# Kernel optimization log

Hardware: AMD Instinct MI355X
Metric: run time of the kernel (lower is better)

Reference implementation:

```python
import jax, jax.numpy as jnp
import numpy as np

# Router hyperparameters (match init_kwargs)
GATE_TEMP = 1.0
Z_LOSS_COEF = 0.01
CAPACITY_FACTOR = 1.25
NUM_SELECTED = 2
NUM_EXPERTS = 64

B, S, D = 4, 8192, 2048


def setup_inputs() -> dict:
    key = jax.random.key(0)
    k1, k2 = jax.random.split(key)
    hidden_states = jax.random.normal(k1, (B, S, D), dtype=jnp.float32)
    # nn.init.normal_(self.gate.weight, mean=0.0, std=0.01)
    gate_weight = jax.random.normal(k2, (NUM_EXPERTS, D), dtype=jnp.float32) * 0.01
    return {"hidden_states": hidden_states, "gate_weight": gate_weight}


def reference(hidden_states, gate_weight):
    b, s, d = hidden_states.shape
    e = gate_weight.shape[0]
    n = b * s  # num_tokens
    x = hidden_states.reshape(n, d)

    # gate linear (no bias), eval mode -> no jitter noise
    gate_logits = (x @ gate_weight.T) / GATE_TEMP          # [n, e]
    gate_probs = jax.nn.softmax(gate_logits, axis=-1)      # [n, e]

    top_k_probs, top_k_indices = jax.lax.top_k(gate_probs, NUM_SELECTED)  # [n, k]
    expert_weights = top_k_probs / (top_k_probs.sum(-1, keepdims=True) + 1e-8)

    # capacity accounting (vectorized bincount instead of per-expert python loop;
    # top-k indices are distinct per token so `any(dim=-1)` == plain count)
    capacity = int(CAPACITY_FACTOR * n / e * NUM_SELECTED)
    expert_counts = jnp.zeros((e,), jnp.float32).at[top_k_indices.reshape(-1)].add(1.0)
    expert_overflow = jnp.maximum(expert_counts - capacity, 0.0).sum()
    capacity_overflow_pct = expert_overflow / n * 100.0

    # auxiliary metrics
    z_loss = jax.scipy.special.logsumexp(gate_logits, axis=-1).mean() * Z_LOSS_COEF
    gate_entropy = -(gate_probs * jnp.log(gate_probs + 1e-10)).sum(-1).mean()
    expert_load = expert_counts / expert_counts.sum()
    expert_load_variance = ((expert_load - 1.0 / e) ** 2).mean()
    routing_confidence = expert_weights.max(-1)  # [n]

    expert_indices = top_k_indices.reshape(b, s, NUM_SELECTED)
    expert_weights = expert_weights.reshape(b, s, NUM_SELECTED)
    return (expert_indices, expert_weights, expert_counts, capacity_overflow_pct,
            z_loss, gate_entropy, expert_load_variance,
            routing_confidence.reshape(b, s))
```

## Files before the change

kernel.cpp:

```cpp
#include <hip/hip_runtime.h>


#define NTOK 32768
#define DDIM 2048
#define NEXP 64
#define NKS 64
#define LG_STRIDE 68

#define OFF_IDX 0
#define OFF_W 65536
#define OFF_CNT 131072
#define OFF_OVF 131136
#define OFF_ZL 131137
#define OFF_ENT 131138
#define OFF_VAR 131139
#define OFF_CONF 131140

#define WS_PLANES_OFF 1024
#define WS_NEEDED (WS_PLANES_OFF + NKS * 8192)

struct RouterWS {
  unsigned int counts[NEXP];
  double z_sum;
  double ent_sum;
};

typedef _Float16 half8 __attribute__((ext_vector_type(8)));
typedef float floatx4 __attribute__((ext_vector_type(4)));

typedef __attribute__((address_space(1))) void v1_t;
typedef __attribute__((address_space(3))) void v3_t;
__device__ __forceinline__ void cp16(const void* g, void* l) {
  __builtin_amdgcn_global_load_lds((v1_t*)g, (v3_t*)l, 16, 0, 0);
}

__global__ void convert_w(const float* __restrict__ w, _Float16* __restrict__ wp) {
  int tid = blockIdx.x * 256 + threadIdx.x;
  int l = tid & 63;
  int t = (tid >> 6) & 3;
  int s = tid >> 8;
  int e = 16 * t + (l & 15);
  int k0 = 32 * s + (l >> 4) * 8;
  const float* src = w + (size_t)e * DDIM + k0;
  half8 h, lo;
#pragma unroll
  for (int i = 0; i < 8; ++i) {
    float v = src[i] * 256.0f;
    _Float16 hh = (_Float16)v;
    h[i] = hh;
    lo[i] = (_Float16)(v - (float)hh);
  }
  size_t base = (size_t)s * 4096 + ((size_t)t * 64 + l) * 8;
  *(half8*)(wp + base) = h;
  *(half8*)(wp + base + 2048) = lo;
}

__global__ __launch_bounds__(256, 2) void router_mfma(
    const float* __restrict__ x, const _Float16* __restrict__ wp,
    float* __restrict__ out, RouterWS* __restrict__ ws) {
  __shared__ _Float16 wlds[2 * 4096];
  __shared__ float lg[64 * LG_STRIDE];
  __shared__ unsigned int hist[NEXP];

  const int tid = threadIdx.x;
  const int l = tid & 63;
  const int wv = __builtin_amdgcn_readfirstlane(tid >> 6);
  const int r = l & 15;
  const int g = l >> 4;

  const int tokb = blockIdx.x * 64;
  const float* xrow = x + (size_t)(tokb + wv * 16 + r) * DDIM + g * 8;

  floatx4 acc[4];
#pragma unroll
  for (int t = 0; t < 4; ++t) {
    floatx4 z = {0.f, 0.f, 0.f, 0.f};
    acc[t] = z;
  }

  float4 xA0 = *(const float4*)(xrow + 0);
  float4 xA1 = *(const float4*)(xrow + 4);
  float4 xB0 = *(const float4*)(xrow + 32);
  float4 xB1 = *(const float4*)(xrow + 36);
  cp16(wp + tid * 8, (void*)&wlds[tid * 8]);
  cp16(wp + 2048 + tid * 8, (void*)&wlds[2048 + tid * 8]);
  __syncthreads();

#define CVT8(X0, X1, XH, XL)                                                   \
  {                                                                            \
    float vv[8] = {X0.x, X0.y, X0.z, X0.w, X1.x, X1.y, X1.z, X1.w};            \
    _Pragma("unroll") for (int i = 0; i < 8; ++i) {                            \
      _Float16 hh = (_Float16)vv[i];                                           \
      XH[i] = hh;                                                              \
      XL[i] = (_Float16)(vv[i] - (float)hh);                                   \
    }                                                                          \
  }

#define STEP(S, CB, NB, X0, X1)                                                \
  {                                                                            \
    const int s_ = (S);                                                        \
    if (s_ + 1 < NKS) {         \
      const _Float16* sp = wp + (size_t)(s_ + 1) * 4096 + tid * 8;             \
      cp16(sp, (void*)&wlds[(NB) + tid * 8]);                                  \
      cp16(sp + 2048, (void*)&wlds[(NB) + 2048 + tid * 8]);                    \
    }                                                                          \
    half8 xh, xl;                                                              \
    CVT8(X0, X1, xh, xl);                                                      \
    if (s_ + 2 < NKS) {           \
      X0 = *(const float4*)(xrow + (s_ + 2) * 32);                             \
      X1 = *(const float4*)(xrow + (s_ + 2) * 32 + 4);                         \
    }                                                                          \
    _Pragma("unroll") for (int t = 0; t < 4; ++t) {                            \
      half8 wh = *(const half8*)&wlds[(CB) + (t * 64 + l) * 8];                \
      half8 wl = *(const half8*)&wlds[(CB) + 2048 + (t * 64 + l) * 8];         \
      acc[t] = __builtin_amdgcn_mfma_f32_16x16x32_f16(xh, wh, acc[t], 0, 0, 0);\
      acc[t] = __builtin_amdgcn_mfma_f32_16x16x32_f16(xh, wl, acc[t], 0, 0, 0);\
      acc[t] = __builtin_amdgcn_mfma_f32_16x16x32_f16(xl, wh, acc[t], 0, 0, 0);\
      acc[t] = __builtin_amdgcn_mfma_f32_16x16x32_f16(xl, wl, acc[t], 0, 0, 0);\
    }                                                                          \
    __syncthreads();                                                           \
  }

  for (int ss = 0; ss < NKS; ss += 2) {
    STEP(ss, 0, 4096, xA0, xA1);
    STEP(ss + 1, 4096, 0, xB0, xB1);
  }
#undef STEP
#undef CVT8

#pragma unroll
  for (int t = 0; t < 4; ++t)
#pragma unroll
    for (int j = 0; j < 4; ++j)
      lg[(wv * 16 + g * 4 + j) * LG_STRIDE + 16 * t + r] = acc[t][j] * 0.00390625f;

  if (tid < NEXP) hist[tid] = 0;
  __syncthreads();

  if (tid < 64) {
    const int t = tid;
    const float* Lg = &lg[t * LG_STRIDE];

    float m1 = Lg[0];
    int i1 = 0;
    for (int e = 1; e < NEXP; ++e) {
      float v = Lg[e];
      if (v > m1) { m1 = v; i1 = e; }
    }
    float m2 = -3.4e38f;
    int i2 = 0;
    for (int e = 0; e < NEXP; ++e) {
      if (e == i1) continue;
      float v = Lg[e];
      if (v > m2) { m2 = v; i2 = e; }
    }

    float s = 0.f;
    for (int e = 0; e < NEXP; ++e) s += expf(Lg[e] - m1);
    float p1 = expf(Lg[i1] - m1) / s;
    float p2 = expf(Lg[i2] - m1) / s;
    float wsum = p1 + p2 + 1e-8f;
    float w1 = p1 / wsum;
    float w2 = p2 / wsum;

    float ent = 0.f;
    for (int e = 0; e < NEXP; ++e) {
      float p = expf(Lg[e] - m1) / s;
      ent -= p * logf(p + 1e-10f);
    }
    float lse = m1 + logf(s);

    size_t gt = (size_t)blockIdx.x * 64 + t;
    out[OFF_IDX + gt * 2 + 0] = (float)i1;
    out[OFF_IDX + gt * 2 + 1] = (float)i2;
    out[OFF_W + gt * 2 + 0] = w1;
    out[OFF_W + gt * 2 + 1] = w2;
    out[OFF_CONF + gt] = fmaxf(w1, w2);

    atomicAdd(&hist[i1], 1u);
    atomicAdd(&hist[i2], 1u);

    float zv = lse, ev = ent;
#pragma unroll
    for (int o = 32; o > 0; o >>= 1) {
      zv += __shfl_down(zv, o);
      ev += __shfl_down(ev, o);
    }
    if (t == 0) {
      atomicAdd(&ws->z_sum, (double)zv);
      atomicAdd(&ws->ent_sum, (double)ev);
    }
  }
  __syncthreads();
  if (tid < NEXP) atomicAdd(&ws->counts[tid], hist[tid]);
}

#define TTILE 128
#define KB 32
#define NCH (DDIM / KB)
#define XSTR 36
#define XBUF (TTILE * XSTR)
#define WBUF (NEXP * XSTR)
#define WOFF (2 * XBUF)

__global__ __launch_bounds__(512, 4) void router_fp32(
    const float* __restrict__ x, const float* __restrict__ w,
    float* __restrict__ out, RouterWS* __restrict__ ws) {
  __shared__ float smem[2 * XBUF + 2 * WBUF];
  __shared__ unsigned int hist[NEXP];

  const int tid = threadIdx.x;
  const int L = tid & 63;
  const int wv = __builtin_amdgcn_readfirstlane(tid >> 6);
  const float* xg = x + (size_t)blockIdx.x * TTILE * DDIM;
  const int sr = tid >> 3;
  const int sc = (tid & 7) * 4;

  float4 rx0 = *(const float4*)(xg + (size_t)sr * DDIM + sc);
  float4 rx1 = *(const float4*)(xg + (size_t)(sr + 64) * DDIM + sc);
  float4 rw = *(const float4*)(w + (size_t)sr * DDIM + sc);
  *(float4*)&smem[sr * XSTR + sc] = rx0;
  *(float4*)&smem[(sr + 64) * XSTR + sc] = rx1;
  *(float4*)&smem[WOFF + sr * XSTR + sc] = rw;

  float acc0[8], acc1[8];
#pragma unroll
  for (int e = 0; e < 8; ++e) { acc0[e] = 0.f; acc1[e] = 0.f; }
  __syncthreads();

  for (int c = 0; c < NCH; ++c) {
    const int cxb = (c & 1) * XBUF;
    const int cwb = WOFF + (c & 1) * WBUF;
    if (c + 1 < NCH) {
      int k0 = (c + 1) * KB;
      rx0 = *(const float4*)(xg + (size_t)sr * DDIM + k0 + sc);
      rx1 = *(const float4*)(xg + (size_t)(sr + 64) * DDIM + k0 + sc);
      rw = *(const float4*)(w + (size_t)sr * DDIM + k0 + sc);
    }
    float4 xr0[8], xr1[8];
#pragma unroll
    for (int m = 0; m < 8; ++m) {
      xr0[m] = *(const float4*)&smem[cxb + L * XSTR + 4 * m];
      xr1[m] = *(const float4*)&smem[cxb + (L + 64) * XSTR + 4 * m];
    }
#pragma unroll
    for (int e = 0; e < 8; ++e) {
      const float* wrow = &smem[cwb + (8 * wv + e) * XSTR];
      float a0 = acc0[e], a1 = acc1[e];
#pragma unroll
      for (int m = 0; m < 8; ++m) {
        float4 wq = *(const float4*)&wrow[4 * m];
        a0 = fmaf(xr0[m].x, wq.x, a0);
        a0 = fmaf(xr0[m].y, wq.y, a0);
        a0 = fmaf(xr0[m].z, wq.z, a0);
        a0 = fmaf(xr0[m].w, wq.w, a0);
        a1 = fmaf(xr1[m].x, wq.x, a1);
        a1 = fmaf(xr1[m].y, wq.y, a1);
        a1 = fmaf(xr1[m].z, wq.z, a1);
        a1 = fmaf(xr1[m].w, wq.w, a1);
      }
      acc0[e] = a0;
      acc1[e] = a1;
    }
    if (c + 1 < NCH) {
      const int nxb = ((c + 1) & 1) * XBUF;
      const int nwb = WOFF + ((c + 1) & 1) * WBUF;
      *(float4*)&smem[nxb + sr * XSTR + sc] = rx0;
      *(float4*)&smem[nxb + (sr + 64) * XSTR + sc] = rx1;
      *(float4*)&smem[nwb + sr * XSTR + sc] = rw;
    }
    __syncthreads();
  }

#pragma unroll
  for (int e = 0; e < 8; ++e) {
    smem[L * LG_STRIDE + wv * 8 + e] = acc0[e];
    smem[(L + 64) * LG_STRIDE + wv * 8 + e] = acc1[e];
  }
  if (tid < NEXP) hist[tid] = 0;
  __syncthreads();

  if (tid < TTILE) {
    const int t = tid;
    const float* Lg = &smem[t * LG_STRIDE];
    float m1 = Lg[0];
    int i1 = 0;
    for (int e = 1; e < NEXP; ++e) {
      float v = Lg[e];
      if (v > m1) { m1 = v; i1 = e; }
    }
    float m2 = -3.4e38f;
    int i2 = 0;
    for (int e = 0; e < NEXP; ++e) {
      if (e == i1) continue;
      float v = Lg[e];
      if (v > m2) { m2 = v; i2 = e; }
    }
    float s = 0.f;
    for (int e = 0; e < NEXP; ++e) s += expf(Lg[e] - m1);
    float p1 = expf(Lg[i1] - m1) / s;
    float p2 = expf(Lg[i2] - m1) / s;
    float wsum = p1 + p2 + 1e-8f;
    float w1 = p1 / wsum;
    float w2 = p2 / wsum;
    float ent = 0.f;
    for (int e = 0; e < NEXP; ++e) {
      float p = expf(Lg[e] - m1) / s;
      ent -= p * logf(p + 1e-10f);
    }
    float lse = m1 + logf(s);
    size_t gt = (size_t)blockIdx.x * TTILE + t;
    out[OFF_IDX + gt * 2 + 0] = (float)i1;
    out[OFF_IDX + gt * 2 + 1] = (float)i2;
    out[OFF_W + gt * 2 + 0] = w1;
    out[OFF_W + gt * 2 + 1] = w2;
    out[OFF_CONF + gt] = fmaxf(w1, w2);
    atomicAdd(&hist[i1], 1u);
    atomicAdd(&hist[i2], 1u);
    float zv = lse, ev = ent;
#pragma unroll
    for (int o = 32; o > 0; o >>= 1) {
      zv += __shfl_down(zv, o);
      ev += __shfl_down(ev, o);
    }
    if ((tid & 63) == 0) {
      atomicAdd(&ws->z_sum, (double)zv);
      atomicAdd(&ws->ent_sum, (double)ev);
    }
  }
  __syncthreads();
  if (tid < NEXP) atomicAdd(&ws->counts[tid], hist[tid]);
}

__global__ void router_final(float* __restrict__ out, RouterWS* __restrict__ ws) {
  int e = threadIdx.x;
  float c = (float)ws->counts[e];
  out[OFF_CNT + e] = c;
  float over = fmaxf(c - 1280.f, 0.f);
  float ld = c / 65536.f - (1.f / 64.f);
  float so = over, sv = ld * ld;
#pragma unroll
  for (int o = 32; o > 0; o >>= 1) {
    so += __shfl_down(so, o);
    sv += __shfl_down(sv, o);
  }
  if (e == 0) {
    out[OFF_OVF] = so / 32768.f * 100.f;
    out[OFF_VAR] = sv / 64.f;
    out[OFF_ZL] = (float)(ws->z_sum / 32768.0 * 0.01);
    out[OFF_ENT] = (float)(ws->ent_sum / 32768.0);
  }
}

extern "C" void kernel_launch(void* const* d_in, const int* in_sizes, int n_in,
                              void* d_out, int out_size, void* d_ws, size_t ws_size,
                              hipStream_t stream) {
  const float* x = (const float*)d_in[0];
  const float* w = (const float*)d_in[1];
  float* out = (float*)d_out;
  RouterWS* ws = (RouterWS*)d_ws;

  (void)hipMemsetAsync(d_ws, 0, sizeof(RouterWS), stream);
  if (ws_size >= (size_t)WS_NEEDED) {
    _Float16* wp = (_Float16*)((char*)d_ws + WS_PLANES_OFF);
    hipLaunchKernelGGL(convert_w, dim3(64), dim3(256), 0, stream, w, wp);
    hipLaunchKernelGGL(router_mfma, dim3(NTOK / 64), dim3(256), 0, stream,
                       x, wp, out, ws);
  } else {
    hipLaunchKernelGGL(router_fp32, dim3(NTOK / TTILE), dim3(512), 0, stream,
                       x, w, out, ws);
  }
  hipLaunchKernelGGL(router_final, dim3(1), dim3(64), 0, stream, out, ws);
}
```

Measured before the change: 89.61 us.

## Load gate weights directly into registers and drop per-step LDS barriers

Instead of staging each K-slice of the packed fp16 weights into LDS with global_load_lds and synchronizing the block every step, each wave now loads its weight fragments straight from global memory into registers, double-buffered across steps. This removes the per-step __syncthreads and the LDS traffic. In exchange, every wave issues its own global loads of the shared weight slice, giving four times the L2/L1 weight traffic, and the two register buffers add about 64 VGPRs, which may strain the launch bound of 2 blocks per CU.

New measurement: 105.0 us. 17.1% more time.

```diff
diff --git a/kernel.cpp b/kernel.cpp
--- a/kernel.cpp
+++ b/kernel.cpp
@@ -27,12 +27,6 @@
 
 typedef _Float16 half8 __attribute__((ext_vector_type(8)));
 typedef float floatx4 __attribute__((ext_vector_type(4)));
-
-typedef __attribute__((address_space(1))) void v1_t;
-typedef __attribute__((address_space(3))) void v3_t;
-__device__ __forceinline__ void cp16(const void* g, void* l) {
-  __builtin_amdgcn_global_load_lds((v1_t*)g, (v3_t*)l, 16, 0, 0);
-}
 
 __global__ void convert_w(const float* __restrict__ w, _Float16* __restrict__ wp) {
   int tid = blockIdx.x * 256 + threadIdx.x;
@@ -58,7 +52,6 @@
 __global__ __launch_bounds__(256, 2) void router_mfma(
     const float* __restrict__ x, const _Float16* __restrict__ wp,
     float* __restrict__ out, RouterWS* __restrict__ ws) {
-  __shared__ _Float16 wlds[2 * 4096];
   __shared__ float lg[64 * LG_STRIDE];
   __shared__ unsigned int hist[NEXP];
 
@@ -70,6 +63,7 @@
 
   const int tokb = blockIdx.x * 64;
   const float* xrow = x + (size_t)(tokb + wv * 16 + r) * DDIM + g * 8;
+  const _Float16* wl8 = wp + (size_t)l * 8;
 
   floatx4 acc[4];
 #pragma unroll
@@ -82,9 +76,12 @@
   float4 xA1 = *(const float4*)(xrow + 4);
   float4 xB0 = *(const float4*)(xrow + 32);
   float4 xB1 = *(const float4*)(xrow + 36);
-  cp16(wp + tid * 8, (void*)&wlds[tid * 8]);
-  cp16(wp + 2048 + tid * 8, (void*)&wlds[2048 + tid * 8]);
-  __syncthreads();
+  half8 wA[8], wB[8];
+#pragma unroll
+  for (int t = 0; t < 4; ++t) {
+    wA[2 * t] = *(const half8*)(wl8 + t * 512);
+    wA[2 * t + 1] = *(const half8*)(wl8 + 2048 + t * 512);
+  }
 
 #define CVT8(X0, X1, XH, XL)                                                   \
   {                                                                            \
@@ -96,13 +93,15 @@
     }                                                                          \
   }
 
-#define STEP(S, CB, NB, X0, X1)                                                \
+#define STEP(S, WCUR, WNXT, X0, X1)                                            \
   {                                                                            \
     const int s_ = (S);                                                        \
-    if (s_ + 1 < NKS) {         \
-      const _Float16* sp = wp + (size_t)(s_ + 1) * 4096 + tid * 8;             \
-      cp16(sp, (void*)&wlds[(NB) + tid * 8]);                                  \
-      cp16(sp + 2048, (void*)&wlds[(NB) + 2048 + tid * 8]);                    \
+    if (s_ + 1 < NKS) {      \
+      const _Float16* sp = wl8 + (size_t)(s_ + 1) * 4096;                      \
+      _Pragma("unroll") for (int t = 0; t < 4; ++t) {                          \
+        WNXT[2 * t] = *(const half8*)(sp + t * 512);                           \
+        WNXT[2 * t + 1] = *(const half8*)(sp + 2048 + t * 512);                \
+      }                                                                        \
     }                                                                          \
     half8 xh, xl;                                                              \
     CVT8(X0, X1, xh, xl);                                                      \
@@ -110,20 +109,21 @@
       X0 = *(const float4*)(xrow + (s_ + 2) * 32);                             \
       X1 = *(const float4*)(xrow + (s_ + 2) * 32 + 4);                         \
     }                                                                          \
-    _Pragma("unroll") for (int t = 0; t < 4; ++t) {                            \
-      half8 wh = *(const half8*)&wlds[(CB) + (t * 64 + l) * 8];                \
-      half8 wl = *(const half8*)&wlds[(CB) + 2048 + (t * 64 + l) * 8];         \
-      acc[t] = __builtin_amdgcn_mfma_f32_16x16x32_f16(xh, wh, acc[t], 0, 0, 0);\
-      acc[t] = __builtin_amdgcn_mfma_f32_16x16x32_f16(xh, wl, acc[t], 0, 0, 0);\
-      acc[t] = __builtin_amdgcn_mfma_f32_16x16x32_f16(xl, wh, acc[t], 0, 0, 0);\
-      acc[t] = __builtin_amdgcn_mfma_f32_16x16x32_f16(xl, wl, acc[t], 0, 0, 0);\
+    _Pragma("unroll") for (int t = 0; t < 4; ++t) {     \
+      acc[t] = __builtin_amdgcn_mfma_f32_16x16x32_f16(xh, WCUR[2 * t],         \
+                                                      acc[t], 0, 0, 0);        \
+      acc[t] = __builtin_amdgcn_mfma_f32_16x16x32_f16(xh, WCUR[2 * t + 1],     \
+                                                      acc[t], 0, 0, 0);        \
+      acc[t] = __builtin_amdgcn_mfma_f32_16x16x32_f16(xl, WCUR[2 * t],         \
+                                                      acc[t], 0, 0, 0);        \
+      acc[t] = __builtin_amdgcn_mfma_f32_16x16x32_f16(xl, WCUR[2 * t + 1],     \
+                                                      acc[t], 0, 0, 0);        \
     }                                                                          \
-    __syncthreads();                                                           \
   }
 
   for (int ss = 0; ss < NKS; ss += 2) {
-    STEP(ss, 0, 4096, xA0, xA1);
-    STEP(ss + 1, 4096, 0, xB0, xB1);
+    STEP(ss, wA, wB, xA0, xA1);
+    STEP(ss + 1, wB, wA, xB0, xB1);
   }
 #undef STEP
 #undef CVT8
```

## Stage x tiles through swizzled LDS with a 4-deep async copy pipeline

Applied to the files above, without the earlier changes.

Activations were previously loaded straight from global memory into registers, two k-steps ahead. They are now copied asynchronously into LDS next to the weight planes, using an XOR-swizzled layout, inside a 4-buffer ring that prefetches 3 stages ahead. Each stage ends with an explicit vmcnt wait plus barrier instead of __syncthreads. The goal is to keep more memory loads in flight and hide global latency for the bandwidth-bound x stream. In exchange, LDS use grows to 64KB per block, which may cap occupancy below the 2 blocks per CU requested by the launch bounds.

Result: faster. 75.12 us, median of 2 (-16.2%).

```diff
diff --git a/kernel.cpp b/kernel.cpp
--- a/kernel.cpp
+++ b/kernel.cpp
@@ -58,8 +58,7 @@
 __global__ __launch_bounds__(256, 2) void router_mfma(
     const float* __restrict__ x, const _Float16* __restrict__ wp,
     float* __restrict__ out, RouterWS* __restrict__ ws) {
-  __shared__ _Float16 wlds[2 * 4096];
-  __shared__ float lg[64 * LG_STRIDE];
+  __shared__ __align__(16) char smem[65536];
   __shared__ unsigned int hist[NEXP];
 
   const int tid = threadIdx.x;
@@ -69,7 +68,19 @@
   const int g = l >> 4;
 
   const int tokb = blockIdx.x * 64;
-  const float* xrow = x + (size_t)(tokb + wv * 16 + r) * DDIM + g * 8;
+  const float* xg = x + (size_t)tokb * DDIM;
+
+  const int srow0 = tid >> 3;
+  const int srow1 = srow0 + 32;
+  const int sj = tid & 7;
+  const size_t gx0 = (size_t)srow0 * DDIM + 4 * (sj ^ (srow0 & 7));
+  const size_t gx1 = (size_t)srow1 * DDIM + 4 * (sj ^ (srow1 & 7));
+
+  const int row = wv * 16 + r;
+  const int rs = row & 7;
+  const int so0 = 16 * (row * 8 + ((2 * g) ^ rs));
+  const int so1 = 16 * (row * 8 + ((2 * g + 1) ^ rs));
+  const int wlo = 16 * l;
 
   floatx4 acc[4];
 #pragma unroll
@@ -78,13 +89,19 @@
     acc[t] = z;
   }
 
-  float4 xA0 = *(const float4*)(xrow + 0);
-  float4 xA1 = *(const float4*)(xrow + 4);
-  float4 xB0 = *(const float4*)(xrow + 32);
-  float4 xB1 = *(const float4*)(xrow + 36);
-  cp16(wp + tid * 8, (void*)&wlds[tid * 8]);
-  cp16(wp + 2048 + tid * 8, (void*)&wlds[2048 + tid * 8]);
-  __syncthreads();
+#define STAGE(S, BUF)                                                          \
+  {                                                                            \
+    char* bb_ = smem + (BUF) * 16384;                                          \
+    cp16(xg + (size_t)(S) * 32 + gx0, bb_ + tid * 16);                         \
+    cp16(xg + (size_t)(S) * 32 + gx1, bb_ + 4096 + tid * 16);                  \
+    const char* wsrc_ = (const char*)wp + (size_t)(S) * 8192 + tid * 16;       \
+    cp16(wsrc_, bb_ + 8192 + tid * 16);                                        \
+    cp16(wsrc_ + 4096, bb_ + 12288 + tid * 16);                                \
+  }
+
+#define WAITBAR(NW)                                                            \
+  asm volatile("s_waitcnt vmcnt(" #NW ")\n\ts_barrier" ::: "memory");          \
+  __builtin_amdgcn_sched_barrier(0);
 
 #define CVT8(X0, X1, XH, XL)                                                   \
   {                                                                            \
@@ -96,45 +113,66 @@
     }                                                                          \
   }
 
-#define STEP(S, CB, NB, X0, X1)                                                \
+#define COMPUTE(BUF)                                                           \
+  const char* bb = smem + (BUF) * 16384;                                       \
+  float4 xq0 = *(const float4*)(bb + so0);                                     \
+  float4 xq1 = *(const float4*)(bb + so1);                                     \
+  half8 xh, xl;                                                                \
+  CVT8(xq0, xq1, xh, xl);                                                      \
+  _Pragma("unroll") for (int t = 0; t < 4; ++t) {                              \
+    half8 wh = *(const half8*)(bb + 8192 + 1024 * t + wlo);                    \
+    half8 wl = *(const half8*)(bb + 12288 + 1024 * t + wlo);                   \
+    acc[t] = __builtin_amdgcn_mfma_f32_16x16x32_f16(xh, wh, acc[t], 0, 0, 0);  \
+    acc[t] = __builtin_amdgcn_mfma_f32_16x16x32_f16(xh, wl, acc[t], 0, 0, 0);  \
+    acc[t] = __builtin_amdgcn_mfma_f32_16x16x32_f16(xl, wh, acc[t], 0, 0, 0);  \
+    acc[t] = __builtin_amdgcn_mfma_f32_16x16x32_f16(xl, wl, acc[t], 0, 0, 0);  \
+  }
+
+#define STEP(S, BUF, NW)                                                       \
   {                                                                            \
-    const int s_ = (S);                                                        \
-    if (s_ + 1 < NKS) {         \
-      const _Float16* sp = wp + (size_t)(s_ + 1) * 4096 + tid * 8;             \
-      cp16(sp, (void*)&wlds[(NB) + tid * 8]);                                  \
-      cp16(sp + 2048, (void*)&wlds[(NB) + 2048 + tid * 8]);                    \
-    }                                                                          \
-    half8 xh, xl;                                                              \
-    CVT8(X0, X1, xh, xl);                                                      \
-    if (s_ + 2 < NKS) {           \
-      X0 = *(const float4*)(xrow + (s_ + 2) * 32);                             \
-      X1 = *(const float4*)(xrow + (s_ + 2) * 32 + 4);                         \
-    }                                                                          \
-    _Pragma("unroll") for (int t = 0; t < 4; ++t) {                            \
-      half8 wh = *(const half8*)&wlds[(CB) + (t * 64 + l) * 8];                \
-      half8 wl = *(const half8*)&wlds[(CB) + 2048 + (t * 64 + l) * 8];         \
-      acc[t] = __builtin_amdgcn_mfma_f32_16x16x32_f16(xh, wh, acc[t], 0, 0, 0);\
-      acc[t] = __builtin_amdgcn_mfma_f32_16x16x32_f16(xh, wl, acc[t], 0, 0, 0);\
-      acc[t] = __builtin_amdgcn_mfma_f32_16x16x32_f16(xl, wh, acc[t], 0, 0, 0);\
-      acc[t] = __builtin_amdgcn_mfma_f32_16x16x32_f16(xl, wl, acc[t], 0, 0, 0);\
-    }                                                                          \
-    __syncthreads();                                                           \
-  }
-
-  for (int ss = 0; ss < NKS; ss += 2) {
-    STEP(ss, 0, 4096, xA0, xA1);
-    STEP(ss + 1, 4096, 0, xB0, xB1);
-  }
+    STAGE((S) + 3, (((S) + 3) & 3));                                           \
+    COMPUTE(BUF)                                                               \
+    WAITBAR(NW)                                                                \
+  }
+#define STEPN(S, BUF, NW)                                  \
+  {                                                                            \
+    COMPUTE(BUF)                                                               \
+    WAITBAR(NW)                                                                \
+  }
+
+  STAGE(0, 0)
+  STAGE(1, 1)
+  STAGE(2, 2)
+  if (tid < NEXP) hist[tid] = 0;
+  WAITBAR(8)
+
+  for (int ss = 0; ss < 60; ss += 4) {
+    STEP(ss, 0, 8)
+    STEP(ss + 1, 1, 8)
+    STEP(ss + 2, 2, 8)
+    STEP(ss + 3, 3, 8)
+  }
+  STEP(60, 0, 8)
+  STEPN(61, 1, 4)
+  STEPN(62, 2, 0)
+  {
+    COMPUTE(3)
+  }
+  __syncthreads();
+
 #undef STEP
+#undef STEPN
+#undef COMPUTE
 #undef CVT8
-
+#undef WAITBAR
+#undef STAGE
+
+  float* lg = (float*)smem;
 #pragma unroll
   for (int t = 0; t < 4; ++t)
 #pragma unroll
     for (int j = 0; j < 4; ++j)
       lg[(wv * 16 + g * 4 + j) * LG_STRIDE + 16 * t + r] = acc[t][j] * 0.00390625f;
-
-  if (tid < NEXP) hist[tid] = 0;
   __syncthreads();
 
   if (tid < 64) {
```

## Deepen weight staging to a 4-buffer pipeline with explicit vmcnt waits

Applied to the files above, without the earlier changes.

Replaces the double-buffered LDS weight staging with a four-slot ring buffer that prefetches three K-steps ahead. Each step ends with a hand-written s_waitcnt on a chosen vmcnt plus s_barrier, so the wait covers only the oldest loads and not all outstanding ones. The logits scratch now reuses the same LDS region, keeping LDS use within the 2-blocks-per-CU budget. This adds latency hiding for the global-to-LDS copies. It relies on exact counts of outstanding vector memory operations, which is fragile if the compiler reorders or splits loads.

New measurement: 82.29 us. 8.2% less time.

```diff
diff --git a/kernel.cpp b/kernel.cpp
--- a/kernel.cpp
+++ b/kernel.cpp
@@ -58,8 +58,7 @@
 __global__ __launch_bounds__(256, 2) void router_mfma(
     const float* __restrict__ x, const _Float16* __restrict__ wp,
     float* __restrict__ out, RouterWS* __restrict__ ws) {
-  __shared__ _Float16 wlds[2 * 4096];
-  __shared__ float lg[64 * LG_STRIDE];
+  __shared__ __align__(16) char smem[32768];
   __shared__ unsigned int hist[NEXP];
 
   const int tid = threadIdx.x;
@@ -70,6 +69,7 @@
 
   const int tokb = blockIdx.x * 64;
   const float* xrow = x + (size_t)(tokb + wv * 16 + r) * DDIM + g * 8;
+  const int wlo = 16 * l;
 
   floatx4 acc[4];
 #pragma unroll
@@ -78,13 +78,25 @@
     acc[t] = z;
   }
 
-  float4 xA0 = *(const float4*)(xrow + 0);
-  float4 xA1 = *(const float4*)(xrow + 4);
-  float4 xB0 = *(const float4*)(xrow + 32);
-  float4 xB1 = *(const float4*)(xrow + 36);
-  cp16(wp + tid * 8, (void*)&wlds[tid * 8]);
-  cp16(wp + 2048 + tid * 8, (void*)&wlds[2048 + tid * 8]);
-  __syncthreads();
+  float4 xA0, xA1, xB0, xB1;
+
+#define XLOAD(S, X0, X1)                                                       \
+  {                                                                            \
+    X0 = *(const float4*)(xrow + (size_t)(S) * 32);                            \
+    X1 = *(const float4*)(xrow + (size_t)(S) * 32 + 4);                        \
+  }
+
+#define WSTAGE(S, WB)                                                          \
+  {                                                                            \
+    char* bb_ = smem + (WB) * 8192;                                            \
+    const char* ws_ = (const char*)wp + (size_t)(S) * 8192 + tid * 16;         \
+    cp16(ws_, bb_ + tid * 16);                                                 \
+    cp16(ws_ + 4096, bb_ + 4096 + tid * 16);                                   \
+  }
+
+#define WAITBAR(NW)                                                            \
+  asm volatile("s_waitcnt vmcnt(" #NW ")\n\ts_barrier" ::: "memory");          \
+  __builtin_amdgcn_sched_barrier(0);
 
 #define CVT8(X0, X1, XH, XL)                                                   \
   {                                                                            \
@@ -96,45 +108,81 @@
     }                                                                          \
   }
 
-#define STEP(S, CB, NB, X0, X1)                                                \
+#define MFMAS(WB, XH, XL)                                                      \
   {                                                                            \
-    const int s_ = (S);                                                        \
-    if (s_ + 1 < NKS) {         \
-      const _Float16* sp = wp + (size_t)(s_ + 1) * 4096 + tid * 8;             \
-      cp16(sp, (void*)&wlds[(NB) + tid * 8]);                                  \
-      cp16(sp + 2048, (void*)&wlds[(NB) + 2048 + tid * 8]);                    \
+    const char* wb_ = smem + (WB) * 8192;                                      \
+    _Pragma("unroll") for (int t = 0; t < 4; ++t) {                            \
+      half8 wh8 = *(const half8*)(wb_ + t * 1024 + wlo);                       \
+      half8 wl8 = *(const half8*)(wb_ + 4096 + t * 1024 + wlo);                \
+      acc[t] =                                                                 \
+          __builtin_amdgcn_mfma_f32_16x16x32_f16(XH, wh8, acc[t], 0, 0, 0);    \
+      acc[t] =                                                                 \
+          __builtin_amdgcn_mfma_f32_16x16x32_f16(XH, wl8, acc[t], 0, 0, 0);    \
+      acc[t] =                                                                 \
+          __builtin_amdgcn_mfma_f32_16x16x32_f16(XL, wh8, acc[t], 0, 0, 0);    \
+      acc[t] =                                                                 \
+          __builtin_amdgcn_mfma_f32_16x16x32_f16(XL, wl8, acc[t], 0, 0, 0);    \
     }                                                                          \
+  }
+
+#define STEP(S, WB, X0, X1, NW)                                                \
+  {                                                                            \
     half8 xh, xl;                                                              \
     CVT8(X0, X1, xh, xl);                                                      \
-    if (s_ + 2 < NKS) {           \
-      X0 = *(const float4*)(xrow + (s_ + 2) * 32);                             \
-      X1 = *(const float4*)(xrow + (s_ + 2) * 32 + 4);                         \
-    }                                                                          \
-    _Pragma("unroll") for (int t = 0; t < 4; ++t) {                            \
-      half8 wh = *(const half8*)&wlds[(CB) + (t * 64 + l) * 8];                \
-      half8 wl = *(const half8*)&wlds[(CB) + 2048 + (t * 64 + l) * 8];         \
-      acc[t] = __builtin_amdgcn_mfma_f32_16x16x32_f16(xh, wh, acc[t], 0, 0, 0);\
-      acc[t] = __builtin_amdgcn_mfma_f32_16x16x32_f16(xh, wl, acc[t], 0, 0, 0);\
-      acc[t] = __builtin_amdgcn_mfma_f32_16x16x32_f16(xl, wh, acc[t], 0, 0, 0);\
-      acc[t] = __builtin_amdgcn_mfma_f32_16x16x32_f16(xl, wl, acc[t], 0, 0, 0);\
-    }                                                                          \
-    __syncthreads();                                                           \
-  }
-
-  for (int ss = 0; ss < NKS; ss += 2) {
-    STEP(ss, 0, 4096, xA0, xA1);
-    STEP(ss + 1, 4096, 0, xB0, xB1);
-  }
+    XLOAD((S) + 2, X0, X1)                                                     \
+    WSTAGE((S) + 3, (((S) + 3) & 3))                                           \
+    MFMAS(WB, xh, xl)                                                          \
+    WAITBAR(NW)                                                                \
+  }
+
+  XLOAD(0, xA0, xA1)
+  XLOAD(1, xB0, xB1)
+  WSTAGE(0, 0)
+  WSTAGE(1, 1)
+  WSTAGE(2, 2)
+  if (tid < NEXP) hist[tid] = 0;
+  WAITBAR(4)
+
+  STEP(0, 0, xA0, xA1, 6)
+  for (int b = 1; b < 58; b += 4) {
+    STEP(b + 0, 1, xB0, xB1, 8)
+    STEP(b + 1, 2, xA0, xA1, 8)
+    STEP(b + 2, 3, xB0, xB1, 8)
+    STEP(b + 3, 0, xA0, xA1, 8)
+  }
+  {
+    half8 xh, xl;
+    CVT8(xB0, xB1, xh, xl);
+    XLOAD(63, xB0, xB1)
+    MFMAS(1, xh, xl)
+    WAITBAR(6)
+  }
+  {
+    half8 xh, xl;
+    CVT8(xA0, xA1, xh, xl);
+    MFMAS(2, xh, xl)
+    WAITBAR(2)
+  }
+  {
+    half8 xh, xl;
+    CVT8(xB0, xB1, xh, xl);
+    MFMAS(3, xh, xl)
+  }
+  __syncthreads();
+
 #undef STEP
+#undef MFMAS
 #undef CVT8
-
+#undef WAITBAR
+#undef WSTAGE
+#undef XLOAD
+
+  float* lg = (float*)smem;
 #pragma unroll
   for (int t = 0; t < 4; ++t)
 #pragma unroll
     for (int j = 0; j < 4; ++j)
       lg[(wv * 16 + g * 4 + j) * LG_STRIDE + 16 * t + r] = acc[t][j] * 0.00390625f;
-
-  if (tid < NEXP) hist[tid] = 0;
   __syncthreads();
 
   if (tid < 64) {
```
